# Performance work log

Hardware: AMD Instinct MI355X
Metric: run time of the kernel (lower is better)

## Reference

```python
import jax, jax.numpy as jnp
import numpy as np

NUM_GRIDS = 32
INPUT_DIM = 32
HIDDEN_DIM = 64
OUTPUT_DIM = 32
BATCH = 4096
INIT_SCALE = 0.1


def _borders_np(n_chunks):
    def inv_cdf(x):
        return np.log(2.0 * x) if x <= 0.5 else -np.log(2.0 * (1.0 - x))
    cs = 1.0 / n_chunks
    b = [inv_cdf(i * cs) for i in range(1, n_chunks)]
    left = b[0] - (b[1] - b[0])
    right = b[-1] + (b[-1] - b[-2])
    return np.array([left] + b + [right], dtype=np.float32)


def setup_inputs() -> dict:
    key = jax.random.key(0)
    k1, k2, k3 = jax.random.split(key, 3)
    Pi, Ph = INPUT_DIM // 2, HIDDEN_DIM // 2
    s0 = INIT_SCALE / np.sqrt(INPUT_DIM)
    s1 = INIT_SCALE / np.sqrt(INPUT_DIM * HIDDEN_DIM / 4)
    x = jax.random.normal(k1, (INPUT_DIM, BATCH), dtype=jnp.float32)
    level0_params = jax.random.uniform(k2, (NUM_GRIDS + 1, NUM_GRIDS + 1, HIDDEN_DIM, Pi),
                                       dtype=jnp.float32, minval=-s0, maxval=s0)
    level1_params = jax.random.uniform(k3, (NUM_GRIDS + 1, NUM_GRIDS + 1, OUTPUT_DIM, Pi, Ph),
                                       dtype=jnp.float32, minval=-s1, maxval=s1)
    b_np = _borders_np(NUM_GRIDS)
    borders = jnp.asarray(b_np)
    inv_chunk_lengths = jnp.asarray(1.0 / (b_np[1:] - b_np[:-1]))
    return {"x": x, "level0_params": level0_params, "level1_params": level1_params,
            "borders": borders, "inv_chunk_lengths": inv_chunk_lengths}


def _laplace_cdf(x):
    e = jnp.exp(-jnp.abs(x))
    return jnp.where(x > 0, 1.0 - 0.5 * e, 0.5 * e)


def _bilinear_interp(x1, x2, borders, inv_len, g):
    # x1, x2: [n_pairs, B]
    s1 = _laplace_cdf(x1) * g
    s2 = _laplace_cdf(x2) * g
    i1 = jnp.clip(s1.astype(jnp.int32), 0, g - 1)
    i2 = jnp.clip(s2.astype(jnp.int32), 0, g - 1)
    d1 = (x1 - borders[i1]) * inv_len[i1]
    d2 = (x2 - borders[i2]) * inv_len[i2]
    i1n = jnp.clip(i1 + 1, 0, g)
    i2n = jnp.clip(i2 + 1, 0, g)
    w00 = (1 - d1) * (1 - d2)
    w01 = (1 - d1) * d2
    w10 = d1 * (1 - d2)
    w11 = d1 * d2
    return i1, i2, i1n, i2n, w00, w01, w10, w11


def reference(x, level0_params, level1_params, borders, inv_chunk_lengths):
    g = NUM_GRIDS
    input_dim, B = x.shape
    Pi = input_dim // 2
    H = level0_params.shape[2]
    Ph = H // 2

    xp = x.reshape(Pi, 2, B)
    i1, i2, i1n, i2n, w00, w01, w10, w11 = _bilinear_interp(
        xp[:, 0], xp[:, 1], borders, inv_chunk_lengths, g)

    # level 0: gather 4 corners per (pair, batch) and weighted-accumulate -> z0 [H, B]
    l0t = jnp.transpose(level0_params, (3, 0, 1, 2))  # [Pi, g+1, g+1, H]
    pa = jnp.arange(Pi)[:, None]
    g00 = l0t[pa, i1, i2]    # [Pi, B, H]
    g01 = l0t[pa, i1, i2n]
    g10 = l0t[pa, i1n, i2]
    g11 = l0t[pa, i1n, i2n]
    z0 = (jnp.einsum('pb,pbh->hb', w00, g00)
          + jnp.einsum('pb,pbh->hb', w01, g01)
          + jnp.einsum('pb,pbh->hb', w10, g10)
          + jnp.einsum('pb,pbh->hb', w11, g11))

    z0p = z0.reshape(Ph, 2, B)
    j1, j2, j1n, j2n, wz00, wz01, wz10, wz11 = _bilinear_interp(
        z0p[:, 0], z0p[:, 1], borders, inv_chunk_lengths, g)

    # exactly as the torch loop (note: only idx1 of x and idxz1 of z are used).
    l1t = jnp.transpose(level1_params, (3, 4, 0, 1, 2))  # [Pi, Ph, g+1, g+1, O]
    xa = jnp.arange(Pi)[:, None, None]
    za = jnp.arange(Ph)[None, :, None]
    I1, I1n = i1[:, None, :], i1n[:, None, :]   # [Pi, 1, B]
    J1, J1n = j1[None, :, :], j1n[None, :, :]   # [1, Ph, B]
    q00 = l1t[xa, za, I1, J1]     # [Pi, Ph, B, O]
    q01 = l1t[xa, za, I1, J1n]
    q10 = l1t[xa, za, I1n, J1]
    q11 = l1t[xa, za, I1n, J1n]
    W00 = w00[:, None, :] * wz00[None, :, :]    # [Pi, Ph, B]
    W01 = w00[:, None, :] * wz10[None, :, :]
    W10 = w10[:, None, :] * wz00[None, :, :]
    W11 = w10[:, None, :] * wz10[None, :, :]
    out = (jnp.einsum('xzb,xzbo->ob', W00, q00)
           + jnp.einsum('xzb,xzbo->ob', W01, q01)
           + jnp.einsum('xzb,xzbo->ob', W10, q10)
           + jnp.einsum('xzb,xzbo->ob', W11, q11))
    return out
```

## Files before the change

kernel.cpp:

```cpp
#include <hip/hip_runtime.h>
#include <hip/hip_fp16.h>

#define NG 32
#define NC 33
#define BATCH 4096

static constexpr size_t T1H_BYTES = 17842176ull * 2;
static constexpr size_t T0F_BYTES = 1115136ull * 4;

__device__ __forceinline__ void interp1(float v, const float* sb, const float* sil,
                                        int& i, float& d) {
    float e = expf(-fabsf(v));
    float s = (v > 0.f) ? (1.f - 0.5f * e) : (0.5f * e);
    s *= (float)NG;
    int ii = (int)s;
    ii = ii < 0 ? 0 : (ii > NG - 1 ? NG - 1 : ii);
    d = (v - sb[ii]) * sil[ii];
    i = ii;
}

__global__ __launch_bounds__(256) void k_transpose(
    const float* __restrict__ L1, const float* __restrict__ L0,
    __half* __restrict__ T1, float* __restrict__ T0)
{
    __shared__ __half hbuf[32 * 514];
    __shared__ float  fbuf[64 * 17];
    const int cell = blockIdx.x;

    const size_t base1 = (size_t)cell * 16384;
    for (int t = threadIdx.x; t < 16384; t += 256) {
        float v = L1[base1 + t];
        int o = t >> 9, r = t & 511;
        hbuf[o * 514 + r] = __float2half(v);
    }
    const size_t base0 = (size_t)cell * 1024;
    for (int t = threadIdx.x; t < 1024; t += 256) {
        int h = t >> 4, p = t & 15;
        fbuf[h * 17 + p] = L0[base0 + t];
    }
    __syncthreads();
    for (int t = threadIdx.x; t < 16384; t += 256) {
        int xz = t >> 5, o = t & 31;
        T1[((size_t)xz * 1089 + cell) * 32 + o] = hbuf[o * 514 + xz];
    }
    for (int t = threadIdx.x; t < 1024; t += 256) {
        int p = t >> 6, h = t & 63;
        T0[((size_t)p * 1089 + cell) * 64 + h] = fbuf[h * 17 + p];
    }
}

__global__ __launch_bounds__(256) void k_prep(
    const float* __restrict__ X, const float* __restrict__ T0,
    const float* __restrict__ borders, const float* __restrict__ invlen,
    int* __restrict__ i1x, float* __restrict__ wx0, float* __restrict__ wx1,
    int* __restrict__ j1z, float* __restrict__ wz0, float* __restrict__ wz1)
{
    __shared__ float sb[33], sil[32];
    __shared__ int   scell[16][4];
    __shared__ float sw[4][16][4];
    __shared__ float sz0[4][64];

    const int tid = threadIdx.x;
    if (tid < 33) sb[tid] = borders[tid];
    if (tid >= 64 && tid < 96) sil[tid - 64] = invlen[tid - 64];
    const int h = tid & 63, bl = tid >> 6;
    const int b = blockIdx.x * 4 + bl;
    __syncthreads();

    if (h < 16) {
        const int p = h;
        float x1 = X[(2 * p) * BATCH + b];
        float x2 = X[(2 * p + 1) * BATCH + b];
        int i1, i2; float d1, d2;
        interp1(x1, sb, sil, i1, d1);
        interp1(x2, sb, sil, i2, d2);
        float w00 = (1.f - d1) * (1.f - d2);
        float w01 = (1.f - d1) * d2;
        float w10 = d1 * (1.f - d2);
        float w11 = d1 * d2;
        scell[p][bl] = i1 * 33 + i2;
        sw[0][p][bl] = w00; sw[1][p][bl] = w01; sw[2][p][bl] = w10; sw[3][p][bl] = w11;
        i1x[p * BATCH + b] = i1;
        wx0[p * BATCH + b] = w00;
        wx1[p * BATCH + b] = w10;
    }
    __syncthreads();

    float acc = 0.f;
#pragma unroll 4
    for (int p = 0; p < 16; ++p) {
        int cell = scell[p][bl];
        unsigned basep = ((unsigned)p * 1089u + (unsigned)cell) * 64u + (unsigned)h;
        float t00 = T0[basep];
        float t01 = T0[basep + 64];
        float t10 = T0[basep + 33 * 64];
        float t11 = T0[basep + 34 * 64];
        acc += sw[0][p][bl] * t00 + sw[1][p][bl] * t01 + sw[2][p][bl] * t10 + sw[3][p][bl] * t11;
    }
    sz0[bl][h] = acc;
    __syncthreads();

    if (tid < 128) {
        const int z = tid & 31, bl2 = tid >> 5;
        const int b2 = blockIdx.x * 4 + bl2;
        float z1 = sz0[bl2][2 * z];
        float z2 = sz0[bl2][2 * z + 1];
        int j1, j2u; float dz1, dz2;
        interp1(z1, sb, sil, j1, dz1);
        interp1(z2, sb, sil, j2u, dz2);
        (void)j2u;
        j1z[z * BATCH + b2] = j1;
        wz0[z * BATCH + b2] = (1.f - dz1) * (1.f - dz2);
        wz1[z * BATCH + b2] = dz1 * (1.f - dz2);
    }
}

__device__ __forceinline__ void accum8(float acc[8], uint4 u, float c) {
    union { unsigned u32; __half2 h2; } cv;
    cv.u32 = u.x; { float2 f = __half22float2(cv.h2); acc[0] = fmaf(c, f.x, acc[0]); acc[1] = fmaf(c, f.y, acc[1]); }
    cv.u32 = u.y; { float2 f = __half22float2(cv.h2); acc[2] = fmaf(c, f.x, acc[2]); acc[3] = fmaf(c, f.y, acc[3]); }
    cv.u32 = u.z; { float2 f = __half22float2(cv.h2); acc[4] = fmaf(c, f.x, acc[4]); acc[5] = fmaf(c, f.y, acc[5]); }
    cv.u32 = u.w; { float2 f = __half22float2(cv.h2); acc[6] = fmaf(c, f.x, acc[6]); acc[7] = fmaf(c, f.y, acc[7]); }
}

__global__ __launch_bounds__(256, 4) void k_main(
    const __half* __restrict__ T1,
    const int* __restrict__ i1x, const float* __restrict__ wx0, const float* __restrict__ wx1,
    const int* __restrict__ j1z, const float* __restrict__ wz0, const float* __restrict__ wz1,
    float* __restrict__ out)
{
    __shared__ int   si1[16][4];
    __shared__ float sx0[16][4], sx1[16][4];
    __shared__ int   sj1[32][4];
    __shared__ float sz0w[32][4], sz1w[32][4];

    const int tid = threadIdx.x;
    const int b0 = blockIdx.x * 4;

    if (tid < 64) {
        int p = tid >> 2, bl = tid & 3;
        int idx = p * BATCH + b0 + bl;
        si1[p][bl] = i1x[idx]; sx0[p][bl] = wx0[idx]; sx1[p][bl] = wx1[idx];
    }
    if (tid < 128) {
        int z = tid >> 2, bl = tid & 3;
        int idx = z * BATCH + b0 + bl;
        sj1[z][bl] = j1z[idx]; sz0w[z][bl] = wz0[idx]; sz1w[z][bl] = wz1[idx];
    }
    __syncthreads();

    const int lane = tid & 63, wid = tid >> 6;
    const int oh = lane & 3;
    const int zs = (lane >> 2) & 7;
    const int xs = lane >> 5;
    const int bl = wid;
    const int b = b0 + bl;

    float acc[8];
#pragma unroll
    for (int k = 0; k < 8; ++k) acc[k] = 0.f;

#pragma unroll 2
    for (int xi = 0; xi < 8; ++xi) {
        const int x = xs * 8 + xi;
        const int i1 = si1[x][bl];
        const float X0 = sx0[x][bl], X1 = sx1[x][bl];
        const int xbase = x * 32;
#pragma unroll
        for (int zi = 0; zi < 4; ++zi) {
            const int z = zs * 4 + zi;
            const int j1 = sj1[z][bl];
            const float Z0 = sz0w[z][bl], Z1 = sz1w[z][bl];
            const unsigned hb = (((unsigned)(xbase + z) * 1089u) + (unsigned)(i1 * 33 + j1)) * 32u
                                + (unsigned)(oh * 8);
            uint4 u00 = *reinterpret_cast<const uint4*>(T1 + hb);
            uint4 u01 = *reinterpret_cast<const uint4*>(T1 + hb + 32);
            uint4 u10 = *reinterpret_cast<const uint4*>(T1 + hb + 33 * 32);
            uint4 u11 = *reinterpret_cast<const uint4*>(T1 + hb + 34 * 32);
            const float c00 = X0 * Z0, c01 = X0 * Z1, c10 = X1 * Z0, c11 = X1 * Z1;
            accum8(acc, u00, c00);
            accum8(acc, u01, c01);
            accum8(acc, u10, c10);
            accum8(acc, u11, c11);
        }
    }

#pragma unroll
    for (int m = 4; m <= 32; m <<= 1) {
#pragma unroll
        for (int k = 0; k < 8; ++k) acc[k] += __shfl_xor(acc[k], m, 64);
    }
    if (lane < 4) {
#pragma unroll
        for (int k = 0; k < 8; ++k) out[(oh * 8 + k) * BATCH + b] = acc[k];
    }
}

extern "C" void kernel_launch(void* const* d_in, const int* in_sizes, int n_in,
                              void* d_out, int out_size, void* d_ws, size_t ws_size,
                              hipStream_t stream) {
    const float* X       = (const float*)d_in[0];
    const float* L0      = (const float*)d_in[1];
    const float* L1      = (const float*)d_in[2];
    const float* borders = (const float*)d_in[3];
    const float* invlen  = (const float*)d_in[4];
    float* out = (float*)d_out;

    char* ws = (char*)d_ws;
    __half* T1h = (__half*)ws;
    float*  T0f = (float*)(ws + T1H_BYTES);
    char* p = ws + T1H_BYTES + T0F_BYTES;
    int*   i1x = (int*)p;            p += 16 * BATCH * 4;
    float* wx0 = (float*)p;          p += 16 * BATCH * 4;
    float* wx1 = (float*)p;          p += 16 * BATCH * 4;
    int*   j1z = (int*)p;            p += 32 * BATCH * 4;
    float* wz0 = (float*)p;          p += 32 * BATCH * 4;
    float* wz1 = (float*)p;          p += 32 * BATCH * 4;

    hipLaunchKernelGGL(k_transpose, dim3(1089), dim3(256), 0, stream, L1, L0, T1h, T0f);
    hipLaunchKernelGGL(k_prep, dim3(BATCH / 4), dim3(256), 0, stream,
                       X, T0f, borders, invlen, i1x, wx0, wx1, j1z, wz0, wz1);
    hipLaunchKernelGGL(k_main, dim3(BATCH / 4), dim3(256), 0, stream,
                       T1h, i1x, wx0, wx1, j1z, wz0, wz1, out);
}
```

Measured before the change: 167.3 us.

## Fuse prep and main kernels, vectorize transpose, accumulate in half2

Merges k_prep and k_main into a single fused kernel, so the per-sample indices and weights stay in shared memory and no longer round-trip through global workspace. The transpose kernel now uses float4 loads, half2 stores to LDS and 16-byte global writes. The main loop assigns the two z-corner columns to different lanes and accumulates with packed half2 FMAs instead of fp32 FMAs. This cuts one launch and the memory traffic between stages, at the cost of lower accumulation precision, which could affect accuracy.

```diff
diff --git a/kernel.cpp b/kernel.cpp
--- a/kernel.cpp
+++ b/kernel.cpp
@@ -2,7 +2,6 @@
 #include <hip/hip_fp16.h>
 
 #define NG 32
-#define NC 33
 #define BATCH 4096
 
 static constexpr size_t T1H_BYTES = 17842176ull * 2;
@@ -23,52 +22,81 @@
     const float* __restrict__ L1, const float* __restrict__ L0,
     __half* __restrict__ T1, float* __restrict__ T0)
 {
-    __shared__ __half hbuf[32 * 514];
+    __shared__ __half hbuf[32 * 516];
     __shared__ float  fbuf[64 * 17];
     const int cell = blockIdx.x;
-
-    const size_t base1 = (size_t)cell * 16384;
-    for (int t = threadIdx.x; t < 16384; t += 256) {
-        float v = L1[base1 + t];
-        int o = t >> 9, r = t & 511;
-        hbuf[o * 514 + r] = __float2half(v);
-    }
-    const size_t base0 = (size_t)cell * 1024;
-    for (int t = threadIdx.x; t < 1024; t += 256) {
+    const int tid = threadIdx.x;
+
+    const float4* L1v = reinterpret_cast<const float4*>(L1 + (size_t)cell * 16384);
+#pragma unroll
+    for (int k = 0; k < 16; ++k) {
+        int v = tid + k * 256;
+        int idx = v * 4;
+        int o = idx >> 9, r = idx & 511;
+        float4 f = L1v[v];
+        *reinterpret_cast<__half2*>(&hbuf[o * 516 + r])     = __float22half2_rn(make_float2(f.x, f.y));
+        *reinterpret_cast<__half2*>(&hbuf[o * 516 + r + 2]) = __float22half2_rn(make_float2(f.z, f.w));
+    }
+    const float* L0s = L0 + (size_t)cell * 1024;
+#pragma unroll
+    for (int k = 0; k < 4; ++k) {
+        int t = tid + k * 256;
         int h = t >> 4, p = t & 15;
-        fbuf[h * 17 + p] = L0[base0 + t];
-    }
-    __syncthreads();
-    for (int t = threadIdx.x; t < 16384; t += 256) {
-        int xz = t >> 5, o = t & 31;
-        T1[((size_t)xz * 1089 + cell) * 32 + o] = hbuf[o * 514 + xz];
-    }
-    for (int t = threadIdx.x; t < 1024; t += 256) {
+        fbuf[h * 17 + p] = L0s[t];
+    }
+    __syncthreads();
+
+#pragma unroll
+    for (int k = 0; k < 8; ++k) {
+        int t = tid + k * 256;
+        int xz = t >> 2, o0 = (t & 3) * 8;
+        __half tmp[8];
+#pragma unroll
+        for (int j = 0; j < 8; ++j) tmp[j] = hbuf[(o0 + j) * 516 + xz];
+        *reinterpret_cast<uint4*>(&T1[((size_t)xz * 1089 + cell) * 32 + o0]) =
+            *reinterpret_cast<const uint4*>(tmp);
+    }
+#pragma unroll
+    for (int k = 0; k < 4; ++k) {
+        int t = tid + k * 256;
         int p = t >> 6, h = t & 63;
         T0[((size_t)p * 1089 + cell) * 64 + h] = fbuf[h * 17 + p];
     }
 }
 
-__global__ __launch_bounds__(256) void k_prep(
+__device__ __forceinline__ void accumh2(__half2 acc[4], uint4 u, __half2 c) {
+    union { unsigned u32; __half2 h2; } cv;
+    cv.u32 = u.x; acc[0] = __hfma2(c, cv.h2, acc[0]);
+    cv.u32 = u.y; acc[1] = __hfma2(c, cv.h2, acc[1]);
+    cv.u32 = u.z; acc[2] = __hfma2(c, cv.h2, acc[2]);
+    cv.u32 = u.w; acc[3] = __hfma2(c, cv.h2, acc[3]);
+}
+
+__global__ __launch_bounds__(256, 4) void k_fused(
     const float* __restrict__ X, const float* __restrict__ T0,
+    const __half* __restrict__ T1,
     const float* __restrict__ borders, const float* __restrict__ invlen,
-    int* __restrict__ i1x, float* __restrict__ wx0, float* __restrict__ wx1,
-    int* __restrict__ j1z, float* __restrict__ wz0, float* __restrict__ wz1)
+    float* __restrict__ out)
 {
     __shared__ float sb[33], sil[32];
     __shared__ int   scell[16][4];
-    __shared__ float sw[4][16][4];
+    __shared__ float ssw[4][16][4];
     __shared__ float sz0[4][64];
+    __shared__ int   si1[16][4];
+    __shared__ float sX0[16][4], sX1[16][4];
+    __shared__ int   sj1[32][4];
+    __shared__ float sZ[2][32][4];
 
     const int tid = threadIdx.x;
+    const int b0 = blockIdx.x * 4;
+
     if (tid < 33) sb[tid] = borders[tid];
     if (tid >= 64 && tid < 96) sil[tid - 64] = invlen[tid - 64];
-    const int h = tid & 63, bl = tid >> 6;
-    const int b = blockIdx.x * 4 + bl;
-    __syncthreads();
-
-    if (h < 16) {
-        const int p = h;
+    __syncthreads();
+
+    if (tid < 64) {
+        const int p = tid & 15, bl = tid >> 4;
+        const int b = b0 + bl;
         float x1 = X[(2 * p) * BATCH + b];
         float x2 = X[(2 * p + 1) * BATCH + b];
         int i1, i2; float d1, d2;
@@ -79,120 +107,88 @@
         float w10 = d1 * (1.f - d2);
         float w11 = d1 * d2;
         scell[p][bl] = i1 * 33 + i2;
-        sw[0][p][bl] = w00; sw[1][p][bl] = w01; sw[2][p][bl] = w10; sw[3][p][bl] = w11;
-        i1x[p * BATCH + b] = i1;
-        wx0[p * BATCH + b] = w00;
-        wx1[p * BATCH + b] = w10;
-    }
-    __syncthreads();
-
-    float acc = 0.f;
+        ssw[0][p][bl] = w00; ssw[1][p][bl] = w01; ssw[2][p][bl] = w10; ssw[3][p][bl] = w11;
+        si1[p][bl] = i1;
+        sX0[p][bl] = w00;
+        sX1[p][bl] = w10;
+    }
+    __syncthreads();
+
+    {
+        const int h = tid & 63, bl = tid >> 6;
+        float acc = 0.f;
 #pragma unroll 4
-    for (int p = 0; p < 16; ++p) {
-        int cell = scell[p][bl];
-        unsigned basep = ((unsigned)p * 1089u + (unsigned)cell) * 64u + (unsigned)h;
-        float t00 = T0[basep];
-        float t01 = T0[basep + 64];
-        float t10 = T0[basep + 33 * 64];
-        float t11 = T0[basep + 34 * 64];
-        acc += sw[0][p][bl] * t00 + sw[1][p][bl] * t01 + sw[2][p][bl] * t10 + sw[3][p][bl] * t11;
-    }
-    sz0[bl][h] = acc;
+        for (int p = 0; p < 16; ++p) {
+            int cell = scell[p][bl];
+            unsigned basep = ((unsigned)p * 1089u + (unsigned)cell) * 64u + (unsigned)h;
+            float t00 = T0[basep];
+            float t01 = T0[basep + 64];
+            float t10 = T0[basep + 33 * 64];
+            float t11 = T0[basep + 34 * 64];
+            acc += ssw[0][p][bl] * t00 + ssw[1][p][bl] * t01 + ssw[2][p][bl] * t10 + ssw[3][p][bl] * t11;
+        }
+        sz0[bl][h] = acc;
+    }
     __syncthreads();
 
     if (tid < 128) {
-        const int z = tid & 31, bl2 = tid >> 5;
-        const int b2 = blockIdx.x * 4 + bl2;
-        float z1 = sz0[bl2][2 * z];
-        float z2 = sz0[bl2][2 * z + 1];
+        const int z = tid & 31, bl = tid >> 5;
+        float z1 = sz0[bl][2 * z];
+        float z2 = sz0[bl][2 * z + 1];
         int j1, j2u; float dz1, dz2;
         interp1(z1, sb, sil, j1, dz1);
         interp1(z2, sb, sil, j2u, dz2);
         (void)j2u;
-        j1z[z * BATCH + b2] = j1;
-        wz0[z * BATCH + b2] = (1.f - dz1) * (1.f - dz2);
-        wz1[z * BATCH + b2] = dz1 * (1.f - dz2);
-    }
-}
-
-__device__ __forceinline__ void accum8(float acc[8], uint4 u, float c) {
-    union { unsigned u32; __half2 h2; } cv;
-    cv.u32 = u.x; { float2 f = __half22float2(cv.h2); acc[0] = fmaf(c, f.x, acc[0]); acc[1] = fmaf(c, f.y, acc[1]); }
-    cv.u32 = u.y; { float2 f = __half22float2(cv.h2); acc[2] = fmaf(c, f.x, acc[2]); acc[3] = fmaf(c, f.y, acc[3]); }
-    cv.u32 = u.z; { float2 f = __half22float2(cv.h2); acc[4] = fmaf(c, f.x, acc[4]); acc[5] = fmaf(c, f.y, acc[5]); }
-    cv.u32 = u.w; { float2 f = __half22float2(cv.h2); acc[6] = fmaf(c, f.x, acc[6]); acc[7] = fmaf(c, f.y, acc[7]); }
-}
-
-__global__ __launch_bounds__(256, 4) void k_main(
-    const __half* __restrict__ T1,
-    const int* __restrict__ i1x, const float* __restrict__ wx0, const float* __restrict__ wx1,
-    const int* __restrict__ j1z, const float* __restrict__ wz0, const float* __restrict__ wz1,
-    float* __restrict__ out)
-{
-    __shared__ int   si1[16][4];
-    __shared__ float sx0[16][4], sx1[16][4];
-    __shared__ int   sj1[32][4];
-    __shared__ float sz0w[32][4], sz1w[32][4];
-
-    const int tid = threadIdx.x;
-    const int b0 = blockIdx.x * 4;
-
-    if (tid < 64) {
-        int p = tid >> 2, bl = tid & 3;
-        int idx = p * BATCH + b0 + bl;
-        si1[p][bl] = i1x[idx]; sx0[p][bl] = wx0[idx]; sx1[p][bl] = wx1[idx];
-    }
-    if (tid < 128) {
-        int z = tid >> 2, bl = tid & 3;
-        int idx = z * BATCH + b0 + bl;
-        sj1[z][bl] = j1z[idx]; sz0w[z][bl] = wz0[idx]; sz1w[z][bl] = wz1[idx];
-    }
-    __syncthreads();
-
-    const int lane = tid & 63, wid = tid >> 6;
+        sj1[z][bl] = j1;
+        sZ[0][z][bl] = (1.f - dz1) * (1.f - dz2);
+        sZ[1][z][bl] = dz1 * (1.f - dz2);
+    }
+    __syncthreads();
+
+    const int lane = tid & 63, bl = tid >> 6;
+    const int b = b0 + bl;
     const int oh = lane & 3;
-    const int zs = (lane >> 2) & 7;
-    const int xs = lane >> 5;
-    const int bl = wid;
-    const int b = b0 + bl;
-
-    float acc[8];
-#pragma unroll
-    for (int k = 0; k < 8; ++k) acc[k] = 0.f;
+    const int jc = (lane >> 2) & 1;
+    const int zs = lane >> 3;
+    const unsigned loff = (unsigned)(jc * 32 + oh * 8);
+
+    __half2 acc2[4];
+#pragma unroll
+    for (int k = 0; k < 4; ++k) acc2[k] = __half2half2(__float2half(0.f));
 
 #pragma unroll 2
-    for (int xi = 0; xi < 8; ++xi) {
-        const int x = xs * 8 + xi;
-        const int i1 = si1[x][bl];
-        const float X0 = sx0[x][bl], X1 = sx1[x][bl];
-        const int xbase = x * 32;
+    for (int x = 0; x < 16; ++x) {
+        const int cb = si1[x][bl] * 33;
+        const float X0 = sX0[x][bl], X1 = sX1[x][bl];
+        const unsigned xzb = (unsigned)(x * 32 + zs * 4) * 1089u;
 #pragma unroll
         for (int zi = 0; zi < 4; ++zi) {
             const int z = zs * 4 + zi;
-            const int j1 = sj1[z][bl];
-            const float Z0 = sz0w[z][bl], Z1 = sz1w[z][bl];
-            const unsigned hb = (((unsigned)(xbase + z) * 1089u) + (unsigned)(i1 * 33 + j1)) * 32u
-                                + (unsigned)(oh * 8);
-            uint4 u00 = *reinterpret_cast<const uint4*>(T1 + hb);
-            uint4 u01 = *reinterpret_cast<const uint4*>(T1 + hb + 32);
-            uint4 u10 = *reinterpret_cast<const uint4*>(T1 + hb + 33 * 32);
-            uint4 u11 = *reinterpret_cast<const uint4*>(T1 + hb + 34 * 32);
-            const float c00 = X0 * Z0, c01 = X0 * Z1, c10 = X1 * Z0, c11 = X1 * Z1;
-            accum8(acc, u00, c00);
-            accum8(acc, u01, c01);
-            accum8(acc, u10, c10);
-            accum8(acc, u11, c11);
+            const unsigned cell = (unsigned)(cb + sj1[z][bl]);
+            const float Zc = sZ[jc][z][bl];
+            const unsigned base = (xzb + (unsigned)zi * 1089u + cell) * 32u + loff;
+            uint4 u0 = *reinterpret_cast<const uint4*>(T1 + base);
+            uint4 u1 = *reinterpret_cast<const uint4*>(T1 + base + 33 * 32);
+            const float c0 = X0 * Zc, c1 = X1 * Zc;
+            accumh2(acc2, u0, __float2half2_rn(c0));
+            accumh2(acc2, u1, __float2half2_rn(c1));
         }
     }
 
+    float accf[8];
+#pragma unroll
+    for (int k = 0; k < 4; ++k) {
+        float2 f = __half22float2(acc2[k]);
+        accf[2 * k] = f.x; accf[2 * k + 1] = f.y;
+    }
 #pragma unroll
     for (int m = 4; m <= 32; m <<= 1) {
 #pragma unroll
-        for (int k = 0; k < 8; ++k) acc[k] += __shfl_xor(acc[k], m, 64);
+        for (int k = 0; k < 8; ++k) accf[k] += __shfl_xor(accf[k], m, 64);
     }
     if (lane < 4) {
 #pragma unroll
-        for (int k = 0; k < 8; ++k) out[(oh * 8 + k) * BATCH + b] = acc[k];
+        for (int k = 0; k < 8; ++k) out[(oh * 8 + k) * BATCH + b] = accf[k];
     }
 }
 
@@ -209,17 +205,8 @@
     char* ws = (char*)d_ws;
     __half* T1h = (__half*)ws;
     float*  T0f = (float*)(ws + T1H_BYTES);
-    char* p = ws + T1H_BYTES + T0F_BYTES;
-    int*   i1x = (int*)p;            p += 16 * BATCH * 4;
-    float* wx0 = (float*)p;          p += 16 * BATCH * 4;
-    float* wx1 = (float*)p;          p += 16 * BATCH * 4;
-    int*   j1z = (int*)p;            p += 32 * BATCH * 4;
-    float* wz0 = (float*)p;          p += 32 * BATCH * 4;
-    float* wz1 = (float*)p;          p += 32 * BATCH * 4;
 
     hipLaunchKernelGGL(k_transpose, dim3(1089), dim3(256), 0, stream, L1, L0, T1h, T0f);
-    hipLaunchKernelGGL(k_prep, dim3(BATCH / 4), dim3(256), 0, stream,
-                       X, T0f, borders, invlen, i1x, wx0, wx1, j1z, wz0, wz1);
-    hipLaunchKernelGGL(k_main, dim3(BATCH / 4), dim3(256), 0, stream,
-                       T1h, i1x, wx0, wx1, j1z, wz0, wz1, out);
-}
+    hipLaunchKernelGGL(k_fused, dim3(BATCH / 4), dim3(256), 0, stream,
+                       X, T0f, T1h, borders, invlen, out);
+}
```

Result: faster. 149.6 us (-10.6%).
